# Kernel tuning notes

Hardware: AMD Instinct MI355X
Metric: run time of the kernel (lower is better)

Reference implementation:

```python
import jax, jax.numpy as jnp
import numpy as np

T_IN, B, H = 12, 65536, 64
T_OUT = 12
OVERLAP = 3


def setup_inputs() -> dict:
    key = jax.random.key(0)
    ks = jax.random.split(key, 9)
    return {
        "encoder_out": jax.random.normal(ks[0], (T_IN, B, H), dtype=jnp.float32),
        "encoder_hid": jax.random.normal(ks[1], (B, H), dtype=jnp.float32),
        "last": jax.random.normal(ks[2], (B, OVERLAP), dtype=jnp.float32),
        # GRUCell params (PyTorch layout: weight_ih (3H, in), weight_hh (3H, H), gate order r,z,n)
        "W_ih": jax.random.normal(ks[3], (3 * H, OVERLAP), dtype=jnp.float32) * 0.1,
        "W_hh": jax.random.normal(ks[4], (3 * H, H), dtype=jnp.float32) * 0.1,
        "b_ih": jax.random.normal(ks[5], (3 * H,), dtype=jnp.float32) * 0.1,
        "b_hh": jax.random.normal(ks[6], (3 * H,), dtype=jnp.float32) * 0.1,
        # Linear hidden -> 1
        "W_lin": jax.random.normal(ks[7], (1, H), dtype=jnp.float32) * 0.1,
        "b_lin": jax.random.normal(ks[8], (1,), dtype=jnp.float32) * 0.1,
    }


def _gru_cell(x, h, W_ih, W_hh, b_ih, b_hh):
    gi = x @ W_ih.T + b_ih  # (B, 3H)
    gh = h @ W_hh.T + b_hh  # (B, 3H)
    i_r, i_z, i_n = jnp.split(gi, 3, axis=-1)
    h_r, h_z, h_n = jnp.split(gh, 3, axis=-1)
    r = jax.nn.sigmoid(i_r + h_r)
    z = jax.nn.sigmoid(i_z + h_z)
    n = jnp.tanh(i_n + r * h_n)
    return (1.0 - z) * n + z * h


def reference(encoder_out, encoder_hid, last, W_ih, W_hh, b_ih, b_hh, W_lin, b_lin):
    def step(carry, _):
        hidden, lst = carry
        # attention over encoder time steps (softmax along time axis 0)
        attn_w = jnp.einsum('tbk,bk->tb', encoder_out, hidden)
        attn_w = jax.nn.softmax(attn_w, axis=0)
        context = jnp.einsum('tbk,tb->bk', encoder_out, attn_w)
        hidden = hidden + context
        hidden = _gru_cell(lst, hidden, W_ih, W_hh, b_ih, b_hh)
        out = hidden @ W_lin.T + b_lin  # (B, 1)
        # torch uses out.detach() when feeding back
        lst = jnp.concatenate([jax.lax.stop_gradient(out), lst[:, :OVERLAP - 1]], axis=-1)
        return (hidden, lst), out

    (_, _), outs = jax.lax.scan(step, (encoder_hid, last), None, length=T_OUT)
    # outs: (T_OUT, B, 1) -> (B, T_OUT), matching torch.cat(decoder_out, dim=-1)
    return jnp.transpose(outs[:, :, 0], (1, 0))
```

## Files before the change

kernel.cpp:

```cpp
#include <hip/hip_runtime.h>


#define TT 12
#define BB 65536
#define HH 64
#define SROW 104

typedef _Float16 half8 __attribute__((ext_vector_type(8)));
typedef _Float16 half4 __attribute__((ext_vector_type(4)));
typedef float    f32x4 __attribute__((ext_vector_type(4)));
typedef float    f32x2 __attribute__((ext_vector_type(2)));

#define L2E 1.44269504088896f

__device__ __forceinline__ float ex2(float x){ return __builtin_amdgcn_exp2f(x); }
__device__ __forceinline__ float sigm(float x){ return 1.0f/(1.0f + ex2(-L2E*x)); }
__device__ __forceinline__ float tanh_(float x){ return 1.0f - 2.0f/(ex2(2.0f*L2E*x)+1.0f); }

#define PIN_A(x) asm volatile("" : "+a"(x))

template<int N>
__device__ __forceinline__ float ror_add(float x){
    int s = __builtin_amdgcn_update_dpp(0, __float_as_int(x), 0x120+N, 0xF, 0xF, false);
    return x + __int_as_float(s);
}
__device__ __forceinline__ float sum16(float x){
    x = ror_add<1>(x); x = ror_add<2>(x); x = ror_add<4>(x); x = ror_add<8>(x);
    return x;
}

__device__ __forceinline__ float max3f(float a, float b, float c){
    return fmaxf(fmaxf(a,b),c);
}

#define MFMA16(A,B,C) __builtin_amdgcn_mfma_f32_16x16x32_f16(A,B,C,0,0,0)

__global__ __launch_bounds__(256, 2)
void decoder_kernel(const float* __restrict__ enc,
                    const float* __restrict__ hid0,
                    const float* __restrict__ last0,
                    const float* __restrict__ Wih,
                    const float* __restrict__ Whh,
                    const float* __restrict__ bih,
                    const float* __restrict__ bhh,
                    const float* __restrict__ Wlin,
                    const float* __restrict__ blin,
                    float* __restrict__ out)
{
    __shared__ __align__(16) _Float16 sHi[16*SROW];
    __shared__ __align__(16) _Float16 sLo[16*SROW];
    __shared__ __align__(16) float    sGh[16*260];

    const int tid  = threadIdx.x;
    const int wv   = tid >> 6;
    const int lane = tid & 63;
    const int q    = lane & 15;
    const int quad = lane >> 4;
    const int m    = wv*4 + quad;
    const size_t b = (size_t)blockIdx.x*16 + m;
    const int jq   = wv*16 + q;

    for (int i = tid; i < 16*SROW; i += 256){
        if ((i % SROW) >= 68){ sHi[i] = (_Float16)0; sLo[i] = (_Float16)0; }
    }

    f32x4 e4[TT];
    #pragma unroll
    for (int t=0;t<TT;++t)
        e4[t] = *(const f32x4*)(enc + ((size_t)t*BB + b)*HH + 4*q);

    f32x4 h = *(const f32x4*)(hid0 + b*HH + 4*q);
    float l0 = last0[b*3+0], l1 = last0[b*3+1], l2 = last0[b*3+2];
    float bl = blin[0];
    f32x4 wl = *(const f32x4*)(Wlin + 4*q);

    half8 bR0h,bR0l,bR1h,bR1l, bZ0h,bZ0l,bZ1h,bZ1l, bN0h,bN0l,bN1h,bN1l;
    {
        #pragma unroll
        for (int g=0; g<3; ++g){
            int row = g*64 + jq;
            #pragma unroll
            for (int kc=0; kc<2; ++kc){
                const float* src = Whh + row*64 + kc*32 + quad*8;
                half8 vh, vl;
                #pragma unroll
                for (int jj=0;jj<8;++jj){
                    float w = src[jj];
                    _Float16 whi = (_Float16)w;
                    vh[jj] = whi;
                    vl[jj] = (_Float16)(w - (float)whi);
                }
                if (g==0){ if(kc==0){bR0h=vh;bR0l=vl;} else {bR1h=vh;bR1l=vl;} }
                else if (g==1){ if(kc==0){bZ0h=vh;bZ0l=vl;} else {bZ1h=vh;bZ1l=vl;} }
                else { if(kc==0){bN0h=vh;bN0l=vl;} else {bN1h=vh;bN1l=vl;} }
            }
        }
    }
    half8 bR2h, bZ2h, bN2h, bI2h;
    #pragma unroll
    for (int jj=0;jj<8;++jj){ bR2h[jj]=(_Float16)0; bZ2h[jj]=(_Float16)0; bN2h[jj]=(_Float16)0; bI2h[jj]=(_Float16)0; }
    if (quad == 0){
        #pragma unroll
        for (int jj=0;jj<3;++jj){
            bR2h[jj] = (_Float16)Wih[(      jq)*3 + jj];
            bZ2h[jj] = (_Float16)Wih[( 64 + jq)*3 + jj];
            bI2h[jj] = (_Float16)Wih[(128 + jq)*3 + jj];
        }
        bR2h[3] = (_Float16)(bih[      jq] + bhh[      jq]);
        bZ2h[3] = (_Float16)(bih[ 64 + jq] + bhh[ 64 + jq]);
        bN2h[3] = (_Float16)(bhh[128 + jq]);
        bI2h[3] = (_Float16)(bih[128 + jq]);
    }

    PIN_A(bR0h); PIN_A(bR0l); PIN_A(bR1h); PIN_A(bR1l);
    PIN_A(bZ0h); PIN_A(bZ0l); PIN_A(bZ1h); PIN_A(bZ1l);
    PIN_A(bN0h); PIN_A(bN0l); PIN_A(bN1h); PIN_A(bN1l);
    PIN_A(bR2h); PIN_A(bZ2h); PIN_A(bN2h); PIN_A(bI2h);

    for (int s=0;s<TT;++s){
        float a[TT];
        #pragma unroll
        for (int t=0;t<TT;++t){
            f32x2 p2 = e4[t].xy * h.xy;
            p2 += e4[t].zw * h.zw;
            a[t] = sum16(p2.x + p2.y);
        }
        float m0 = max3f(a[0],a[1],a[2]),  m1 = max3f(a[3],a[4],a[5]);
        float m2 = max3f(a[6],a[7],a[8]),  m3 = max3f(a[9],a[10],a[11]);
        float mx = fmaxf(max3f(m0,m1,m2), m3);
        float nm = -mx*L2E;
        #pragma unroll
        for (int t=0;t<TT;++t) a[t] = ex2(__builtin_fmaf(a[t], L2E, nm));
        float s01=a[0]+a[1], s23=a[2]+a[3], s45=a[4]+a[5], s67=a[6]+a[7], s89=a[8]+a[9], sab=a[10]+a[11];
        float ss = ((s01+s23)+(s45+s67)) + (s89+sab);
        float inv = 1.0f/ss;
        f32x4 ctxA = {0.f,0.f,0.f,0.f}, ctxB = {0.f,0.f,0.f,0.f};
        #pragma unroll
        for (int t=0;t<TT;t+=2){
            ctxA += e4[t]   * (f32x4)(a[t]);
            ctxB += e4[t+1] * (f32x4)(a[t+1]);
        }
        h += (ctxA + ctxB) * (f32x4)(inv);

        half4 hhi, hlo;
        #pragma unroll
        for (int j=0;j<4;++j){
            _Float16 hh = (_Float16)h[j];
            hhi[j] = hh;
            hlo[j] = (_Float16)(h[j] - (float)hh);
        }
        *(half4*)&sHi[m*SROW + 4*q] = hhi;
        *(half4*)&sLo[m*SROW + 4*q] = hlo;
        if (q == 0){
            _Float16 a0=(_Float16)l0, a1=(_Float16)l1, a2=(_Float16)l2;
            half4 th = {a0, a1, a2, (_Float16)1.0f};
            half4 tl = {(_Float16)(l0-(float)a0), (_Float16)(l1-(float)a1),
                        (_Float16)(l2-(float)a2), (_Float16)0.0f};
            *(half4*)&sHi[m*SROW + 64] = th;
            *(half4*)&sLo[m*SROW + 64] = tl;
        }
        __syncthreads();

        half8 ahi0 = *(half8*)&sHi[q*SROW +  0 + quad*8];
        half8 ahi1 = *(half8*)&sHi[q*SROW + 32 + quad*8];
        half8 ahi2 = *(half8*)&sHi[q*SROW + 64 + quad*8];
        half8 alo0 = *(half8*)&sLo[q*SROW +  0 + quad*8];
        half8 alo1 = *(half8*)&sLo[q*SROW + 32 + quad*8];
        half8 alo2 = *(half8*)&sLo[q*SROW + 64 + quad*8];

        {
            f32x4 acc = {0.f,0.f,0.f,0.f};
            acc = MFMA16(ahi0,bR0h,acc); acc = MFMA16(ahi1,bR1h,acc);
            acc = MFMA16(ahi0,bR0l,acc); acc = MFMA16(ahi1,bR1l,acc);
            acc = MFMA16(alo0,bR0h,acc); acc = MFMA16(alo1,bR1h,acc);
            acc = MFMA16(ahi2,bR2h,acc); acc = MFMA16(alo2,bR2h,acc);
            #pragma unroll
            for (int r=0;r<4;++r) sGh[(quad*4+r)*260 +   0 + jq] = acc[r];
        }
        {
            f32x4 acc = {0.f,0.f,0.f,0.f};
            acc = MFMA16(ahi0,bZ0h,acc); acc = MFMA16(ahi1,bZ1h,acc);
            acc = MFMA16(ahi0,bZ0l,acc); acc = MFMA16(ahi1,bZ1l,acc);
            acc = MFMA16(alo0,bZ0h,acc); acc = MFMA16(alo1,bZ1h,acc);
            acc = MFMA16(ahi2,bZ2h,acc); acc = MFMA16(alo2,bZ2h,acc);
            #pragma unroll
            for (int r=0;r<4;++r) sGh[(quad*4+r)*260 +  64 + jq] = acc[r];
        }
        {
            f32x4 acc = {0.f,0.f,0.f,0.f};
            acc = MFMA16(ahi0,bN0h,acc); acc = MFMA16(ahi1,bN1h,acc);
            acc = MFMA16(ahi0,bN0l,acc); acc = MFMA16(ahi1,bN1l,acc);
            acc = MFMA16(alo0,bN0h,acc); acc = MFMA16(alo1,bN1h,acc);
            acc = MFMA16(ahi2,bN2h,acc);
            #pragma unroll
            for (int r=0;r<4;++r) sGh[(quad*4+r)*260 + 128 + jq] = acc[r];
        }
        {
            f32x4 acc = {0.f,0.f,0.f,0.f};
            acc = MFMA16(ahi2,bI2h,acc); acc = MFMA16(alo2,bI2h,acc);
            #pragma unroll
            for (int r=0;r<4;++r) sGh[(quad*4+r)*260 + 192 + jq] = acc[r];
        }
        __syncthreads();

        f32x4 gR  = *(f32x4*)&sGh[m*260 +   0 + 4*q];
        f32x4 gZ  = *(f32x4*)&sGh[m*260 +  64 + 4*q];
        f32x4 gNH = *(f32x4*)&sGh[m*260 + 128 + 4*q];
        f32x4 gNI = *(f32x4*)&sGh[m*260 + 192 + 4*q];

        float o = 0.f;
        #pragma unroll
        for (int j=0;j<4;++j){
            float r = sigm(gR[j]);
            float z = sigm(gZ[j]);
            float n = tanh_(gNI[j] + r*gNH[j]);
            float hn = (1.f - z)*n + z*h[j];
            h[j] = hn;
            o += hn * wl[j];
        }
        o = sum16(o) + bl;
        if (q == 0) out[b*TT + s] = o;
        l2 = l1; l1 = l0; l0 = o;
    }
}

extern "C" void kernel_launch(void* const* d_in, const int* in_sizes, int n_in,
                              void* d_out, int out_size, void* d_ws, size_t ws_size,
                              hipStream_t stream)
{
    const float* enc  = (const float*)d_in[0];
    const float* hid0 = (const float*)d_in[1];
    const float* lst  = (const float*)d_in[2];
    const float* Wih  = (const float*)d_in[3];
    const float* Whh  = (const float*)d_in[4];
    const float* bih  = (const float*)d_in[5];
    const float* bhh  = (const float*)d_in[6];
    const float* Wlin = (const float*)d_in[7];
    const float* blin = (const float*)d_in[8];
    decoder_kernel<<<BB/16, 256, 0, stream>>>(enc, hid0, lst, Wih, Whh, bih, bhh,
                                              Wlin, blin, (float*)d_out);
}
```

Measured before the change: 465.3 us.

## Apply GRU gate nonlinearities in MFMA output layout and exchange hidden via LDS

The GRU gate activations and hidden update are now computed directly on the MFMA accumulator registers, in the transposed layout. Before, all four gate matrices were written to a large LDS buffer and read back in row layout. The new hidden state goes to a small fp32 LDS array, which the next step reads back to compute the output projection and feedback. The bias is split into hi/lo fp16 halves using an extra ones column for precision, and launch bounds are raised to 3 blocks per CU with the AGPR pinning removed. This shrinks LDS traffic and footprint to allow more occupancy, at the cost of strided scalar LDS accesses and possible register pressure.

```diff
diff --git a/kernel.cpp b/kernel.cpp
--- a/kernel.cpp
+++ b/kernel.cpp
@@ -5,6 +5,7 @@
 #define BB 65536
 #define HH 64
 #define SROW 104
+#define HFS 65
 
 typedef _Float16 half8 __attribute__((ext_vector_type(8)));
 typedef _Float16 half4 __attribute__((ext_vector_type(4)));
@@ -17,8 +18,6 @@
 __device__ __forceinline__ float sigm(float x){ return 1.0f/(1.0f + ex2(-L2E*x)); }
 __device__ __forceinline__ float tanh_(float x){ return 1.0f - 2.0f/(ex2(2.0f*L2E*x)+1.0f); }
 
-#define PIN_A(x) asm volatile("" : "+a"(x))
-
 template<int N>
 __device__ __forceinline__ float ror_add(float x){
     int s = __builtin_amdgcn_update_dpp(0, __float_as_int(x), 0x120+N, 0xF, 0xF, false);
@@ -35,7 +34,7 @@
 
 #define MFMA16(A,B,C) __builtin_amdgcn_mfma_f32_16x16x32_f16(A,B,C,0,0,0)
 
-__global__ __launch_bounds__(256, 2)
+__global__ __launch_bounds__(256, 3)
 void decoder_kernel(const float* __restrict__ enc,
                     const float* __restrict__ hid0,
                     const float* __restrict__ last0,
@@ -49,7 +48,7 @@
 {
     __shared__ __align__(16) _Float16 sHi[16*SROW];
     __shared__ __align__(16) _Float16 sLo[16*SROW];
-    __shared__ __align__(16) float    sGh[16*260];
+    __shared__ __align__(16) float    sHf[16*HFS];
 
     const int tid  = threadIdx.x;
     const int wv   = tid >> 6;
@@ -59,10 +58,10 @@
     const int m    = wv*4 + quad;
     const size_t b = (size_t)blockIdx.x*16 + m;
     const int jq   = wv*16 + q;
-
-    for (int i = tid; i < 16*SROW; i += 256){
-        if ((i % SROW) >= 68){ sHi[i] = (_Float16)0; sLo[i] = (_Float16)0; }
-    }
+    const int grow = quad*4;
+
+    for (int i = tid; i < 16*SROW; i += 256)
+        if ((i % SROW) >= 69){ sHi[i] = (_Float16)0; sLo[i] = (_Float16)0; }
 
     f32x4 e4[TT];
     #pragma unroll
@@ -96,28 +95,38 @@
             }
         }
     }
-    half8 bR2h, bZ2h, bN2h, bI2h;
+    half8 bR2, bZ2, bN2, bI2;
     #pragma unroll
-    for (int jj=0;jj<8;++jj){ bR2h[jj]=(_Float16)0; bZ2h[jj]=(_Float16)0; bN2h[jj]=(_Float16)0; bI2h[jj]=(_Float16)0; }
+    for (int jj=0;jj<8;++jj){ bR2[jj]=(_Float16)0; bZ2[jj]=(_Float16)0; bN2[jj]=(_Float16)0; bI2[jj]=(_Float16)0; }
     if (quad == 0){
         #pragma unroll
         for (int jj=0;jj<3;++jj){
-            bR2h[jj] = (_Float16)Wih[(      jq)*3 + jj];
-            bZ2h[jj] = (_Float16)Wih[( 64 + jq)*3 + jj];
-            bI2h[jj] = (_Float16)Wih[(128 + jq)*3 + jj];
-        }
-        bR2h[3] = (_Float16)(bih[      jq] + bhh[      jq]);
-        bZ2h[3] = (_Float16)(bih[ 64 + jq] + bhh[ 64 + jq]);
-        bN2h[3] = (_Float16)(bhh[128 + jq]);
-        bI2h[3] = (_Float16)(bih[128 + jq]);
-    }
-
-    PIN_A(bR0h); PIN_A(bR0l); PIN_A(bR1h); PIN_A(bR1l);
-    PIN_A(bZ0h); PIN_A(bZ0l); PIN_A(bZ1h); PIN_A(bZ1l);
-    PIN_A(bN0h); PIN_A(bN0l); PIN_A(bN1h); PIN_A(bN1l);
-    PIN_A(bR2h); PIN_A(bZ2h); PIN_A(bN2h); PIN_A(bI2h);
+            bR2[jj] = (_Float16)Wih[(      jq)*3 + jj];
+            bZ2[jj] = (_Float16)Wih[( 64 + jq)*3 + jj];
+            bI2[jj] = (_Float16)Wih[(128 + jq)*3 + jj];
+        }
+        float br = bih[      jq] + bhh[      jq];
+        float bz = bih[ 64 + jq] + bhh[ 64 + jq];
+        float bn = bhh[128 + jq];
+        float bi = bih[128 + jq];
+        _Float16 brh=(_Float16)br, bzh=(_Float16)bz, bnh=(_Float16)bn, bih_=(_Float16)bi;
+        bR2[3]=brh; bR2[4]=(_Float16)(br-(float)brh);
+        bZ2[3]=bzh; bZ2[4]=(_Float16)(bz-(float)bzh);
+        bN2[3]=bnh; bN2[4]=(_Float16)(bn-(float)bnh);
+        bI2[3]=bih_; bI2[4]=(_Float16)(bi-(float)bih_);
+    }
 
     for (int s=0;s<TT;++s){
+        if (s > 0){
+            h[0] = sHf[m*HFS + 4*q + 0];
+            h[1] = sHf[m*HFS + 4*q + 1];
+            h[2] = sHf[m*HFS + 4*q + 2];
+            h[3] = sHf[m*HFS + 4*q + 3];
+            float o = h[0]*wl[0] + h[1]*wl[1] + h[2]*wl[2] + h[3]*wl[3];
+            o = sum16(o) + bl;
+            if (q == 0) out[b*TT + (s-1)] = o;
+            l2 = l1; l1 = l0; l0 = o;
+        }
         float a[TT];
         #pragma unroll
         for (int t=0;t<TT;++t){
@@ -151,6 +160,10 @@
         }
         *(half4*)&sHi[m*SROW + 4*q] = hhi;
         *(half4*)&sLo[m*SROW + 4*q] = hlo;
+        sHf[m*HFS + 4*q + 0] = h[0];
+        sHf[m*HFS + 4*q + 1] = h[1];
+        sHf[m*HFS + 4*q + 2] = h[2];
+        sHf[m*HFS + 4*q + 3] = h[3];
         if (q == 0){
             _Float16 a0=(_Float16)l0, a1=(_Float16)l1, a2=(_Float16)l2;
             half4 th = {a0, a1, a2, (_Float16)1.0f};
@@ -158,6 +171,8 @@
                         (_Float16)(l2-(float)a2), (_Float16)0.0f};
             *(half4*)&sHi[m*SROW + 64] = th;
             *(half4*)&sLo[m*SROW + 64] = tl;
+            sHi[m*SROW + 68] = (_Float16)1.0f;
+            sLo[m*SROW + 68] = (_Float16)0.0f;
         }
         __syncthreads();
 
@@ -168,59 +183,52 @@
         half8 alo1 = *(half8*)&sLo[q*SROW + 32 + quad*8];
         half8 alo2 = *(half8*)&sLo[q*SROW + 64 + quad*8];
 
-        {
-            f32x4 acc = {0.f,0.f,0.f,0.f};
-            acc = MFMA16(ahi0,bR0h,acc); acc = MFMA16(ahi1,bR1h,acc);
-            acc = MFMA16(ahi0,bR0l,acc); acc = MFMA16(ahi1,bR1l,acc);
-            acc = MFMA16(alo0,bR0h,acc); acc = MFMA16(alo1,bR1h,acc);
-            acc = MFMA16(ahi2,bR2h,acc); acc = MFMA16(alo2,bR2h,acc);
-            #pragma unroll
-            for (int r=0;r<4;++r) sGh[(quad*4+r)*260 +   0 + jq] = acc[r];
-        }
-        {
-            f32x4 acc = {0.f,0.f,0.f,0.f};
-            acc = MFMA16(ahi0,bZ0h,acc); acc = MFMA16(ahi1,bZ1h,acc);
-            acc = MFMA16(ahi0,bZ0l,acc); acc = MFMA16(ahi1,bZ1l,acc);
-            acc = MFMA16(alo0,bZ0h,acc); acc = MFMA16(alo1,bZ1h,acc);
-            acc = MFMA16(ahi2,bZ2h,acc); acc = MFMA16(alo2,bZ2h,acc);
-            #pragma unroll
-            for (int r=0;r<4;++r) sGh[(quad*4+r)*260 +  64 + jq] = acc[r];
-        }
-        {
-            f32x4 acc = {0.f,0.f,0.f,0.f};
-            acc = MFMA16(ahi0,bN0h,acc); acc = MFMA16(ahi1,bN1h,acc);
-            acc = MFMA16(ahi0,bN0l,acc); acc = MFMA16(ahi1,bN1l,acc);
-            acc = MFMA16(alo0,bN0h,acc); acc = MFMA16(alo1,bN1h,acc);
-            acc = MFMA16(ahi2,bN2h,acc);
-            #pragma unroll
-            for (int r=0;r<4;++r) sGh[(quad*4+r)*260 + 128 + jq] = acc[r];
-        }
-        {
-            f32x4 acc = {0.f,0.f,0.f,0.f};
-            acc = MFMA16(ahi2,bI2h,acc); acc = MFMA16(alo2,bI2h,acc);
-            #pragma unroll
-            for (int r=0;r<4;++r) sGh[(quad*4+r)*260 + 192 + jq] = acc[r];
+        f32x4 accR = {0.f,0.f,0.f,0.f};
+        accR = MFMA16(ahi0,bR0h,accR); accR = MFMA16(ahi1,bR1h,accR);
+        accR = MFMA16(ahi0,bR0l,accR); accR = MFMA16(ahi1,bR1l,accR);
+        accR = MFMA16(alo0,bR0h,accR); accR = MFMA16(alo1,bR1h,accR);
+        accR = MFMA16(ahi2,bR2 ,accR); accR = MFMA16(alo2,bR2 ,accR);
+
+        f32x4 accZ = {0.f,0.f,0.f,0.f};
+        accZ = MFMA16(ahi0,bZ0h,accZ); accZ = MFMA16(ahi1,bZ1h,accZ);
+        accZ = MFMA16(ahi0,bZ0l,accZ); accZ = MFMA16(ahi1,bZ1l,accZ);
+        accZ = MFMA16(alo0,bZ0h,accZ); accZ = MFMA16(alo1,bZ1h,accZ);
+        accZ = MFMA16(ahi2,bZ2 ,accZ); accZ = MFMA16(alo2,bZ2 ,accZ);
+
+        f32x4 accN = {0.f,0.f,0.f,0.f};
+        accN = MFMA16(ahi0,bN0h,accN); accN = MFMA16(ahi1,bN1h,accN);
+        accN = MFMA16(ahi0,bN0l,accN); accN = MFMA16(ahi1,bN1l,accN);
+        accN = MFMA16(alo0,bN0h,accN); accN = MFMA16(alo1,bN1h,accN);
+        accN = MFMA16(ahi2,bN2 ,accN);
+
+        f32x4 accI = {0.f,0.f,0.f,0.f};
+        accI = MFMA16(ahi2,bI2 ,accI); accI = MFMA16(alo2,bI2 ,accI);
+
+        float hA0 = sHf[(grow+0)*HFS + jq];
+        float hA1 = sHf[(grow+1)*HFS + jq];
+        float hA2 = sHf[(grow+2)*HFS + jq];
+        float hA3 = sHf[(grow+3)*HFS + jq];
+        float hAv[4] = {hA0,hA1,hA2,hA3};
+
+        #pragma unroll
+        for (int r=0;r<4;++r){
+            float rg = sigm(accR[r]);
+            float zg = sigm(accZ[r]);
+            float ng = tanh_(accI[r] + rg*accN[r]);
+            float hn = (1.f - zg)*ng + zg*hAv[r];
+            sHf[(grow+r)*HFS + jq] = hn;
         }
         __syncthreads();
-
-        f32x4 gR  = *(f32x4*)&sGh[m*260 +   0 + 4*q];
-        f32x4 gZ  = *(f32x4*)&sGh[m*260 +  64 + 4*q];
-        f32x4 gNH = *(f32x4*)&sGh[m*260 + 128 + 4*q];
-        f32x4 gNI = *(f32x4*)&sGh[m*260 + 192 + 4*q];
-
-        float o = 0.f;
-        #pragma unroll
-        for (int j=0;j<4;++j){
-            float r = sigm(gR[j]);
-            float z = sigm(gZ[j]);
-            float n = tanh_(gNI[j] + r*gNH[j]);
-            float hn = (1.f - z)*n + z*h[j];
-            h[j] = hn;
-            o += hn * wl[j];
-        }
+    }
+
+    {
+        float h0 = sHf[m*HFS + 4*q + 0];
+        float h1 = sHf[m*HFS + 4*q + 1];
+        float h2 = sHf[m*HFS + 4*q + 2];
+        float h3 = sHf[m*HFS + 4*q + 3];
+        float o = h0*wl[0] + h1*wl[1] + h2*wl[2] + h3*wl[3];
         o = sum16(o) + bl;
-        if (q == 0) out[b*TT + s] = o;
-        l2 = l1; l1 = l0; l0 = o;
+        if (q == 0) out[b*TT + 11] = o;
     }
 }
 
```

Measured after the change: 455.1 us. -2.2%, faster.
